# Kernel tuning notes

Measured on AMD Instinct MI355X. Metric: run time of the kernel, lower is better.

The kernel has to match this reference:

```python
import jax, jax.numpy as jnp
import numpy as np

B, S, SD, CD, F, H = 64, 2048, 32, 8, 1024, 512
D = CD + 1  # lstm input size


def _uinit(k, shape, fan_in):
    lim = 1.0 / np.sqrt(fan_in)
    return jax.random.uniform(k, shape, minval=-lim, maxval=lim, dtype=jnp.float32)


def setup_inputs() -> dict:
    key = jax.random.key(0)
    ks = jax.random.split(key, 12)
    return {
        "initial_state": jax.random.normal(ks[0], (B, SD), dtype=jnp.float32),
        "rnn_input": jax.random.normal(ks[1], (B, S, D), dtype=jnp.float32),
        # encoder MLP: in->H, H->H, H->F (equinox MLP depth=2, relu hidden, identity final)
        "enc_w0": _uinit(ks[2], (H, SD), SD), "enc_b0": _uinit(ks[3], (H,), SD),
        "enc_w1": _uinit(ks[4], (H, H), H), "enc_b1": _uinit(ks[5], (H,), H),
        "enc_w2": _uinit(ks[6], (F, H), H), "enc_b2": _uinit(ks[7], (F,), H),
        # equinox LSTMCell params: weight_ih (4F,D), weight_hh (4F,F), bias (4F,)
        "w_ih": _uinit(ks[8], (4 * F, D), F), "w_hh": _uinit(ks[9], (4 * F, F), F),
        "bias": _uinit(ks[10], (4 * F,), F),
    }


def reference(initial_state, rnn_input, enc_w0, enc_b0, enc_w1, enc_b1, enc_w2, enc_b2, w_ih, w_hh, bias):
    # encoder MLP -> initial hidden state
    h0 = jax.nn.relu(initial_state @ enc_w0.T + enc_b0)
    h0 = jax.nn.relu(h0 @ enc_w1.T + enc_b1)
    h0 = h0 @ enc_w2.T + enc_b2              # [B, F]
    c0 = jnp.zeros_like(h0)

    xs = jnp.swapaxes(rnn_input, 0, 1)       # [S, B, D]

    def step(carry, x):
        h, c = carry
        lin = x @ w_ih.T + h @ w_hh.T + bias  # [B, 4F]
        i, f, g, o = jnp.split(lin, 4, axis=-1)
        c_new = jax.nn.sigmoid(f) * c + jax.nn.sigmoid(i) * jnp.tanh(g)
        h_new = jax.nn.sigmoid(o) * jnp.tanh(c_new)
        # emit the PRE-step hidden state, matching `(self.cell(input, state), state[0])`
        return (h_new, c_new), h

    (h_last, _), h_seq = jax.lax.scan(step, (h0, c0), xs)
    return h_last, jnp.swapaxes(h_seq, 0, 1)  # [B,F], [B,S,F]
```

## Files before the change

kernel.cpp:

```cpp
#include <hip/hip_runtime.h>
#include <hip/hip_bf16.h>
#include <cstdint>
#include <cstddef>


typedef __bf16 bf16x8_t __attribute__((ext_vector_type(8)));
typedef float f32x4_t __attribute__((ext_vector_type(4)));
typedef int   i32x4_t __attribute__((ext_vector_type(4)));
typedef unsigned long long u64_t;
typedef unsigned long long u64x2_t __attribute__((ext_vector_type(2)));
typedef unsigned short u16x4_t __attribute__((ext_vector_type(4)));

#define WS_TAGS    0
#define WS_HBUF    1048576
#define WS_WSHUF   1310720
#define WS_WAUG    9699328
#define WS_XHAT    9961472
#define WS_H1      18350080
#define WS_H2      18481152

__device__ __forceinline__ unsigned short f2bf(float f) {
  unsigned int u = __float_as_uint(f);
  u = (u + 0x7fffu + ((u >> 16) & 1u)) >> 16;
  return (unsigned short)u;
}
__device__ __forceinline__ float sigm(float x) { return 1.f / (1.f + __expf(-x)); }
__device__ __forceinline__ float tanh_f(float x) {
  float e = __expf(-2.f * fabsf(x));
  float r = (1.f - e) / (1.f + e);
  return copysignf(r, x);
}


__global__ void flumen_enc1(const float* __restrict__ x, const float* __restrict__ W,
                            const float* __restrict__ b, float* __restrict__ h1) {
  const int bb = blockIdx.x;
  const int o  = threadIdx.x;
  const f32x4_t* xr = (const f32x4_t*)(x + bb * 32);
  const f32x4_t* wr = (const f32x4_t*)(W + o * 32);
  float acc = b[o];
#pragma unroll
  for (int q = 0; q < 8; ++q) {
    f32x4_t xv = xr[q], wv = wr[q];
    acc += xv[0] * wv[0] + xv[1] * wv[1] + xv[2] * wv[2] + xv[3] * wv[3];
  }
  h1[bb * 512 + o] = fmaxf(acc, 0.f);
}

__global__ void flumen_enc2(const float* __restrict__ in, const float* __restrict__ W,
                            const float* __restrict__ bv, float* __restrict__ outb) {
  __shared__ float s[64 * 256];
  const int tid = threadIdx.x;
  const int ol = tid & 63, bg = tid >> 6;
  const int o = blockIdx.x * 64 + ol;
  float bias = bv[o];
  float acc[8];
#pragma unroll
  for (int q = 0; q < 8; ++q) acc[q] = bias;
  for (int p = 0; p < 2; ++p) {
    __syncthreads();
    for (int i = tid; i < 4096; i += 512) {
      int flat = i * 4;
      int bb = flat >> 8, kk = flat & 255;
      *(f32x4_t*)(s + flat) = *(const f32x4_t*)(in + bb * 512 + p * 256 + kk);
    }
    __syncthreads();
    for (int kk = 0; kk < 256; kk += 4) {
      f32x4_t wv = *(const f32x4_t*)(W + o * 512 + p * 256 + kk);
#pragma unroll
      for (int j = 0; j < 4; ++j) {
        float wj = wv[j];
#pragma unroll
        for (int q = 0; q < 8; ++q)
          acc[q] += wj * s[(bg * 8 + q) * 256 + kk + j];
      }
    }
  }
#pragma unroll
  for (int q = 0; q < 8; ++q)
    outb[(bg * 8 + q) * 512 + o] = fmaxf(acc[q], 0.f);
}

__global__ void flumen_enc3(const float* __restrict__ in, const float* __restrict__ W,
                            const float* __restrict__ bv, float* __restrict__ dout,
                            unsigned short* __restrict__ hbuf) {
  __shared__ float s[64 * 256];
  const int tid = threadIdx.x;
  const int ol = tid & 63, bg = tid >> 6;
  const int o = blockIdx.x * 64 + ol;
  float bias = bv[o];
  float acc[8];
#pragma unroll
  for (int q = 0; q < 8; ++q) acc[q] = bias;
  for (int p = 0; p < 2; ++p) {
    __syncthreads();
    for (int i = tid; i < 4096; i += 512) {
      int flat = i * 4;
      int bb = flat >> 8, kk = flat & 255;
      *(f32x4_t*)(s + flat) = *(const f32x4_t*)(in + bb * 512 + p * 256 + kk);
    }
    __syncthreads();
    for (int kk = 0; kk < 256; kk += 4) {
      f32x4_t wv = *(const f32x4_t*)(W + o * 512 + p * 256 + kk);
#pragma unroll
      for (int j = 0; j < 4; ++j) {
        float wj = wv[j];
#pragma unroll
        for (int q = 0; q < 8; ++q)
          acc[q] += wj * s[(bg * 8 + q) * 256 + kk + j];
      }
    }
  }
  float* out_hseq = dout + 65536;
#pragma unroll
  for (int q = 0; q < 8; ++q) {
    int bb = bg * 8 + q;
    float v = acc[q];
    out_hseq[(size_t)bb * 2097152 + o] = v;
    int blk  = (bb >> 4) * 32 + (o >> 5);
    int lane = ((o >> 3) & 3) * 16 + (bb & 15);
    hbuf[blk * 512 + lane * 8 + (o & 7)] = f2bf(v);
  }
}


__global__ void flumen_wshuf(const float* __restrict__ src, unsigned short* __restrict__ dst) {
  int idx = blockIdx.x * 512 + threadIdx.x;
  int lane = idx & 63, kt = (idx >> 6) & 31, mt = idx >> 11;
  int r = lane & 15;
  int g = r & 3, f = mt * 4 + (r >> 2);
  int k0 = kt * 32 + (lane >> 4) * 8;
  const float* sp = src + (size_t)(g * 1024 + f) * 1024 + k0;
  f32x4_t v0 = *(const f32x4_t*)(sp);
  f32x4_t v1 = *(const f32x4_t*)(sp + 4);
  u16x4_t o0, o1;
#pragma unroll
  for (int j = 0; j < 4; ++j) { o0[j] = f2bf(v0[j]); o1[j] = f2bf(v1[j]); }
  u16x4_t* dp = (u16x4_t*)(dst + (size_t)idx * 8);
  dp[0] = o0; dp[1] = o1;
}

__global__ void flumen_waugi(const float* __restrict__ wih, const float* __restrict__ bias,
                             unsigned short* __restrict__ dst) {
  int idx = blockIdx.x * 512 + threadIdx.x;
  int lane = idx & 63, mt = idx >> 6;
  int r = lane & 15;
  int g = r & 3, f = mt * 4 + (r >> 2);
  int k0 = (lane >> 4) * 8;
  unsigned short o[8];
#pragma unroll
  for (int j = 0; j < 8; ++j) {
    int k = k0 + j;
    float v = (k < 9) ? wih[(size_t)(g * 1024 + f) * 9 + k]
                      : (k == 9 ? bias[g * 1024 + f] : 0.f);
    o[j] = f2bf(v);
  }
  u16x4_t* dp = (u16x4_t*)(dst + (size_t)idx * 8);
  dp[0] = *(u16x4_t*)&o[0];
  dp[1] = *(u16x4_t*)&o[4];
}

__global__ void flumen_convx(const float* __restrict__ xin, unsigned short* __restrict__ dst) {
  int i = (blockIdx.x * 512 + threadIdx.x) * 4;
  int b = i >> 16, t = (i >> 5) & 2047, c0 = i & 31;
  u16x4_t o;
#pragma unroll
  for (int j = 0; j < 4; ++j) {
    int cc = c0 + j;
    float v = (cc < 9) ? xin[((size_t)b * 2048 + t) * 9 + cc] : (cc == 9 ? 1.f : 0.f);
    o[j] = f2bf(v);
  }
  *(u16x4_t*)(dst + ((size_t)t * 64 + b) * 32 + c0) = o;
}

__global__ __launch_bounds__(512, 1) void flumen_lstm(
    const unsigned short* __restrict__ Wshuf,
    const unsigned short* __restrict__ WaugI,
    const unsigned short* __restrict__ Xhat,
    unsigned short* hbuf, int* tags, float* out)
{
  __shared__ __align__(16) char smem[140288];
  char*  h_lds = smem;
  float* hs    = (float*)(smem + 131072);
  float* pbuf  = (float*)smem;

  float* out_hlast = out;
  float* out_hseq  = out + 65536;
  const int w    = blockIdx.x;
  const int tid  = threadIdx.x;
  const int lane = tid & 63;
  const int wave = tid >> 6;
  const int mtp  = wave & 3;
  const int kh   = wave >> 2;
  const int l15  = lane & 15;
  const int l4   = lane >> 4;

  bf16x8_t Apin[2][16];
#pragma unroll
  for (int mtl = 0; mtl < 2; ++mtl) {
    const char* ap = (const char*)Wshuf + (size_t)(w * 8 + mtp * 2 + mtl) * 32768
                   + (size_t)(kh * 16) * 1024 + lane * 16;
#pragma unroll
    for (int k16 = 0; k16 < 16; ++k16)
      Apin[mtl][k16] = *(const bf16x8_t*)(ap + k16 * 1024);
  }
  bf16x8_t wfragI[2];
#pragma unroll
  for (int mtl = 0; mtl < 2; ++mtl)
    wfragI[mtl] = *(const bf16x8_t*)((const char*)WaugI
                                     + (size_t)(w * 8 + mtp * 2 + mtl) * 1024 + lane * 16);

  float carr[2][4] = {{0.f,0.f,0.f,0.f},{0.f,0.f,0.f,0.f}};

  for (int t = 0; t < 2048; ++t) {
    f32x4_t acc[2][4];
    if (kh == 0) {
#pragma unroll
      for (int n = 0; n < 4; ++n) {
        const int batch = n * 16 + l15;
        bf16x8_t xf = *(const bf16x8_t*)(Xhat + ((size_t)t * 64 + batch) * 32 + l4 * 8);
#pragma unroll
        for (int mtl = 0; mtl < 2; ++mtl)
          acc[mtl][n] = __builtin_amdgcn_mfma_f32_16x16x32_bf16(
              wfragI[mtl], xf, (f32x4_t){0.f, 0.f, 0.f, 0.f}, 0, 0, 0);
      }
    } else {
#pragma unroll
      for (int mtl = 0; mtl < 2; ++mtl)
#pragma unroll
        for (int n = 0; n < 4; ++n)
          acc[mtl][n] = (f32x4_t){0.f, 0.f, 0.f, 0.f};
    }

    if (t > 0) {
      if (lane < 32) {
        const char* tp = (const char*)tags + ((size_t)(t - 1) * 32 + lane) * 16;
        int iter = 0;
        while (true) {
          i32x4_t tv;
          asm volatile("global_load_dwordx4 %0, %1, off sc1\n\ts_waitcnt vmcnt(0)"
                       : "=v"(tv) : "v"(tp) : "memory");
          bool good = (tv[0] == t) && (tv[1] == t) && (tv[2] == t) && (tv[3] == t);
          if (__all(good) || ++iter >= (1 << 20)) break;
        }
      }
      __builtin_amdgcn_sched_barrier(0);
    }

    {
      const char* src0 = (const char*)hbuf + (size_t)((t & 1) * 131072) + tid * 16;
      f32x4_t v[8];
#pragma unroll
      for (int i = 0; i < 8; ++i)
        asm volatile("global_load_dwordx4 %0, %1, off sc1"
                     : "=v"(v[i]) : "v"(src0 + i * 8192) : "memory");
      asm volatile("s_waitcnt vmcnt(0)" ::: "memory");
      __builtin_amdgcn_sched_barrier(0);
#pragma unroll
      for (int i = 0; i < 8; ++i)
        *(f32x4_t*)(h_lds + tid * 16 + i * 8192) = v[i];
#pragma unroll
      for (int i = 0; i < 8; ++i)
        asm volatile("global_load_dwordx4 %0, %1, off sc1"
                     : "=v"(v[i]) : "v"(src0 + (i + 8) * 8192) : "memory");
      asm volatile("s_waitcnt vmcnt(0)" ::: "memory");
      __builtin_amdgcn_sched_barrier(0);
#pragma unroll
      for (int i = 0; i < 8; ++i)
        *(f32x4_t*)(h_lds + tid * 16 + (i + 8) * 8192) = v[i];
    }
    __syncthreads();

#pragma unroll
    for (int n = 0; n < 4; ++n) {
      const char* bb = h_lds + (size_t)(n * 32 + kh * 16) * 1024 + lane * 16;
#pragma unroll
      for (int k16 = 0; k16 < 16; ++k16) {
        bf16x8_t bf = *(const bf16x8_t*)(bb + k16 * 1024);
        acc[0][n] = __builtin_amdgcn_mfma_f32_16x16x32_bf16(Apin[0][k16], bf, acc[0][n], 0, 0, 0);
        acc[1][n] = __builtin_amdgcn_mfma_f32_16x16x32_bf16(Apin[1][k16], bf, acc[1][n], 0, 0, 0);
      }
    }
    __syncthreads();

    if (kh == 1) {
#pragma unroll
      for (int mtl = 0; mtl < 2; ++mtl)
#pragma unroll
        for (int n = 0; n < 4; ++n)
          *(f32x4_t*)(pbuf + ((size_t)((mtp * 8 + mtl * 4 + n) * 64) + lane) * 4)
              = acc[mtl][n];
    }
    __syncthreads();

    if (kh == 0) {
#pragma unroll
      for (int mtl = 0; mtl < 2; ++mtl)
#pragma unroll
        for (int n = 0; n < 4; ++n) {
          f32x4_t p = *(const f32x4_t*)(pbuf + ((size_t)((mtp * 8 + mtl * 4 + n) * 64) + lane) * 4);
          f32x4_t s = acc[mtl][n] + p;
          const int batch = n * 16 + l15;
          float c = sigm(s[1]) * carr[mtl][n] + sigm(s[0]) * tanh_f(s[2]);
          carr[mtl][n] = c;
          float h = sigm(s[3]) * tanh_f(c);
          const int fl = (mtp * 2 + mtl) * 4 + l4;
          if (t < 2047) {
            hs[batch * 36 + fl] = h;
          } else {
            out_hlast[batch * 1024 + w * 32 + fl] = h;
          }
        }
    }
    __syncthreads();

    if (t < 2047) {
      if (kh == 1) {
        const int b = mtp * 16 + l15;
        const float* hp = hs + b * 36 + l4 * 8;
        f32x4_t u0 = *(const f32x4_t*)(hp);
        f32x4_t u1 = *(const f32x4_t*)(hp + 4);
        u64_t lo = (u64_t)f2bf(u0[0]) | ((u64_t)f2bf(u0[1]) << 16)
                 | ((u64_t)f2bf(u0[2]) << 32) | ((u64_t)f2bf(u0[3]) << 48);
        u64_t hi = (u64_t)f2bf(u1[0]) | ((u64_t)f2bf(u1[1]) << 16)
                 | ((u64_t)f2bf(u1[2]) << 32) | ((u64_t)f2bf(u1[3]) << 48);
        u64x2_t qv = {lo, hi};
        char* dst = (char*)hbuf + (size_t)(((t + 1) & 1) * 131072)
                  + (size_t)(mtp * 32 + w) * 1024 + lane * 16;
        asm volatile("global_store_dwordx4 %0, %1, off sc1" :: "v"(dst), "v"(qv) : "memory");
        asm volatile("s_waitcnt vmcnt(0)" ::: "memory");
        if (lane == 0) {
          int val = t + 1;
          char* tp = (char*)tags + ((size_t)t * 32 + w) * 16 + mtp * 4;
          asm volatile("global_store_dword %0, %1, off sc1" :: "v"(tp), "v"(val) : "memory");
        }
      } else {
        const int b2 = mtp * 16 + (lane >> 2), sg = lane & 3;
        float* hd = out_hseq + ((size_t)b2 * 2048 + (size_t)(t + 1)) * 1024 + w * 32 + sg * 8;
        *(f32x4_t*)hd       = *(const f32x4_t*)(hs + b2 * 36 + sg * 8);
        *(f32x4_t*)(hd + 4) = *(const f32x4_t*)(hs + b2 * 36 + sg * 8 + 4);
      }
    }
  }
}


extern "C" void kernel_launch(void* const* d_in, const int* in_sizes, int n_in,
                              void* d_out, int out_size, void* d_ws, size_t ws_size,
                              hipStream_t stream) {
  const float* initial_state = (const float*)d_in[0];
  const float* rnn_input     = (const float*)d_in[1];
  const float* enc_w0        = (const float*)d_in[2];
  const float* enc_b0        = (const float*)d_in[3];
  const float* enc_w1        = (const float*)d_in[4];
  const float* enc_b1        = (const float*)d_in[5];
  const float* enc_w2        = (const float*)d_in[6];
  const float* enc_b2        = (const float*)d_in[7];
  const float* w_ih          = (const float*)d_in[8];
  const float* w_hh          = (const float*)d_in[9];
  const float* bias          = (const float*)d_in[10];

  char* ws = (char*)d_ws;
  int*            tags  = (int*)(ws + WS_TAGS);
  unsigned short* hbuf  = (unsigned short*)(ws + WS_HBUF);
  unsigned short* Wshuf = (unsigned short*)(ws + WS_WSHUF);
  unsigned short* WaugI = (unsigned short*)(ws + WS_WAUG);
  unsigned short* Xhat  = (unsigned short*)(ws + WS_XHAT);
  float*          h1    = (float*)(ws + WS_H1);
  float*          h2    = (float*)(ws + WS_H2);
  float*          out   = (float*)d_out;

  (void)hipMemsetAsync(tags, 0, 1048576, stream);
  flumen_enc1<<<64, 512, 0, stream>>>(initial_state, enc_w0, enc_b0, h1);
  flumen_enc2<<<8, 512, 0, stream>>>(h1, enc_w1, enc_b1, h2);
  flumen_enc3<<<16, 512, 0, stream>>>(h2, enc_w2, enc_b2, out, hbuf);
  flumen_wshuf<<<1024, 512, 0, stream>>>(w_hh, Wshuf);
  flumen_waugi<<<32, 512, 0, stream>>>(w_ih, bias, WaugI);
  flumen_convx<<<2048, 512, 0, stream>>>(rnn_input, Xhat);
  flumen_lstm<<<32, 512, 0, stream>>>(Wshuf, WaugI, Xhat, hbuf, tags, out);
}
```

Before: 18.40 ms.

## Replace tag flags with parity-encoded h data and pipeline per batch group

Removes the separate tag array and its polling: each block now spins directly on the hidden-state data, whose validity comes from a parity bit pattern XORed into the bf16 values (bit 14 flipped on alternating step pairs), and a scrub kernel pre-fills the buffers. The recurrent step is split into four 16-batch chunks, and the next chunk's h load is issued before the current chunk's MFMAs to overlap latency. This avoids a store-then-flag round trip and the waitcnt before the flag store, at the cost of more barriers per step and a validity check that depends on real h values never matching the sentinel bits.

```diff
diff --git a/kernel.cpp b/kernel.cpp
--- a/kernel.cpp
+++ b/kernel.cpp
@@ -6,18 +6,19 @@
 
 typedef __bf16 bf16x8_t __attribute__((ext_vector_type(8)));
 typedef float f32x4_t __attribute__((ext_vector_type(4)));
-typedef int   i32x4_t __attribute__((ext_vector_type(4)));
+typedef unsigned int u32x4_t __attribute__((ext_vector_type(4)));
 typedef unsigned long long u64_t;
 typedef unsigned long long u64x2_t __attribute__((ext_vector_type(2)));
 typedef unsigned short u16x4_t __attribute__((ext_vector_type(4)));
 
-#define WS_TAGS    0
-#define WS_HBUF    1048576
-#define WS_WSHUF   1310720
-#define WS_WAUG    9699328
-#define WS_XHAT    9961472
-#define WS_H1      18350080
-#define WS_H2      18481152
+#define WS_HBUF    0
+#define WS_WSHUF   393216
+#define WS_WAUG    8781824
+#define WS_XHAT    9043968
+#define WS_H1      17432576
+#define WS_H2      17563648
+
+#define PAR_M 0x40004000u
 
 __device__ __forceinline__ unsigned short f2bf(float f) {
   unsigned int u = __float_as_uint(f);
@@ -123,6 +124,12 @@
   }
 }
 
+
+__global__ void flumen_scrub(unsigned int* __restrict__ hb) {
+  int i = blockIdx.x * 512 + threadIdx.x;
+  u32x4_t pat = {PAR_M, 0u, PAR_M, 0u};
+  *(u32x4_t*)(hb + 32768 + i * 4) = pat;
+}
 
 __global__ void flumen_wshuf(const float* __restrict__ src, unsigned short* __restrict__ dst) {
   int idx = blockIdx.x * 512 + threadIdx.x;
@@ -177,12 +184,12 @@
     const unsigned short* __restrict__ Wshuf,
     const unsigned short* __restrict__ WaugI,
     const unsigned short* __restrict__ Xhat,
-    unsigned short* hbuf, int* tags, float* out)
+    unsigned short* hbuf, float* out)
 {
-  __shared__ __align__(16) char smem[140288];
+  __shared__ __align__(16) char smem[148480];
   char*  h_lds = smem;
   float* hs    = (float*)(smem + 131072);
-  float* pbuf  = (float*)smem;
+  float* pbuf  = (float*)(smem + 140288);
 
   float* out_hlast = out;
   float* out_hseq  = out + 65536;
@@ -212,133 +219,131 @@
 
   float carr[2][4] = {{0.f,0.f,0.f,0.f},{0.f,0.f,0.f,0.f}};
 
+  u32x4_t v[4];
+  {
+    const char* src = (const char*)hbuf + tid * 16;
+#pragma unroll
+    for (int i = 0; i < 4; ++i)
+      asm volatile("global_load_dwordx4 %0, %1, off sc1"
+                   : "=v"(v[i]) : "v"(src + i * 8192) : "memory");
+  }
+
   for (int t = 0; t < 2048; ++t) {
-    f32x4_t acc[2][4];
-    if (kh == 0) {
-#pragma unroll
-      for (int n = 0; n < 4; ++n) {
-        const int batch = n * 16 + l15;
-        bf16x8_t xf = *(const bf16x8_t*)(Xhat + ((size_t)t * 64 + batch) * 32 + l4 * 8);
-#pragma unroll
-        for (int mtl = 0; mtl < 2; ++mtl)
-          acc[mtl][n] = __builtin_amdgcn_mfma_f32_16x16x32_bf16(
-              wfragI[mtl], xf, (f32x4_t){0.f, 0.f, 0.f, 0.f}, 0, 0, 0);
-      }
-    } else {
-#pragma unroll
-      for (int mtl = 0; mtl < 2; ++mtl)
-#pragma unroll
-        for (int n = 0; n < 4; ++n)
-          acc[mtl][n] = (f32x4_t){0.f, 0.f, 0.f, 0.f};
-    }
-
-    if (t > 0) {
-      if (lane < 32) {
-        const char* tp = (const char*)tags + ((size_t)(t - 1) * 32 + lane) * 16;
+    const unsigned p  = (unsigned)((t >> 1) & 1);
+    const bool checkp = (t > 0);
+    const unsigned pm = (checkp && p) ? PAR_M : 0u;
+
+    for (int j = 0; j < 4; ++j) {
+      asm volatile("s_waitcnt vmcnt(0)" ::: "memory");
+      if (checkp) {
+        const char* src = (const char*)hbuf + (size_t)(131072 * (1 + (t & 1)))
+                        + j * 32768 + tid * 16;
         int iter = 0;
         while (true) {
-          i32x4_t tv;
-          asm volatile("global_load_dwordx4 %0, %1, off sc1\n\ts_waitcnt vmcnt(0)"
-                       : "=v"(tv) : "v"(tp) : "memory");
-          bool good = (tv[0] == t) && (tv[1] == t) && (tv[2] == t) && (tv[3] == t);
-          if (__all(good) || ++iter >= (1 << 20)) break;
+          unsigned a = 0xFFFFFFFFu, o = 0u;
+#pragma unroll
+          for (int i = 0; i < 4; ++i)
+#pragma unroll
+            for (int d = 0; d < 4; ++d) { a &= v[i][d]; o |= v[i][d]; }
+          bool valid = p ? ((a & PAR_M) == PAR_M) : ((o & PAR_M) == 0u);
+          if (__all(valid) || ++iter >= (1 << 18)) break;
+#pragma unroll
+          for (int i = 0; i < 4; ++i)
+            asm volatile("global_load_dwordx4 %0, %1, off sc1"
+                         : "=v"(v[i]) : "v"(src + i * 8192) : "memory");
+          asm volatile("s_waitcnt vmcnt(0)" ::: "memory");
         }
       }
       __builtin_amdgcn_sched_barrier(0);
-    }
-
-    {
-      const char* src0 = (const char*)hbuf + (size_t)((t & 1) * 131072) + tid * 16;
-      f32x4_t v[8];
-#pragma unroll
-      for (int i = 0; i < 8; ++i)
-        asm volatile("global_load_dwordx4 %0, %1, off sc1"
-                     : "=v"(v[i]) : "v"(src0 + i * 8192) : "memory");
-      asm volatile("s_waitcnt vmcnt(0)" ::: "memory");
-      __builtin_amdgcn_sched_barrier(0);
-#pragma unroll
-      for (int i = 0; i < 8; ++i)
-        *(f32x4_t*)(h_lds + tid * 16 + i * 8192) = v[i];
-#pragma unroll
-      for (int i = 0; i < 8; ++i)
-        asm volatile("global_load_dwordx4 %0, %1, off sc1"
-                     : "=v"(v[i]) : "v"(src0 + (i + 8) * 8192) : "memory");
-      asm volatile("s_waitcnt vmcnt(0)" ::: "memory");
-      __builtin_amdgcn_sched_barrier(0);
-#pragma unroll
-      for (int i = 0; i < 8; ++i)
-        *(f32x4_t*)(h_lds + tid * 16 + (i + 8) * 8192) = v[i];
-    }
-    __syncthreads();
-
-#pragma unroll
-    for (int n = 0; n < 4; ++n) {
-      const char* bb = h_lds + (size_t)(n * 32 + kh * 16) * 1024 + lane * 16;
-#pragma unroll
-      for (int k16 = 0; k16 < 16; ++k16) {
-        bf16x8_t bf = *(const bf16x8_t*)(bb + k16 * 1024);
-        acc[0][n] = __builtin_amdgcn_mfma_f32_16x16x32_bf16(Apin[0][k16], bf, acc[0][n], 0, 0, 0);
-        acc[1][n] = __builtin_amdgcn_mfma_f32_16x16x32_bf16(Apin[1][k16], bf, acc[1][n], 0, 0, 0);
-      }
-    }
-    __syncthreads();
-
-    if (kh == 1) {
-#pragma unroll
-      for (int mtl = 0; mtl < 2; ++mtl)
-#pragma unroll
-        for (int n = 0; n < 4; ++n)
-          *(f32x4_t*)(pbuf + ((size_t)((mtp * 8 + mtl * 4 + n) * 64) + lane) * 4)
-              = acc[mtl][n];
-    }
-    __syncthreads();
-
-    if (kh == 0) {
-#pragma unroll
-      for (int mtl = 0; mtl < 2; ++mtl)
-#pragma unroll
-        for (int n = 0; n < 4; ++n) {
-          f32x4_t p = *(const f32x4_t*)(pbuf + ((size_t)((mtp * 8 + mtl * 4 + n) * 64) + lane) * 4);
-          f32x4_t s = acc[mtl][n] + p;
-          const int batch = n * 16 + l15;
-          float c = sigm(s[1]) * carr[mtl][n] + sigm(s[0]) * tanh_f(s[2]);
-          carr[mtl][n] = c;
+      {
+        u32x4_t pmv = {pm, pm, pm, pm};
+#pragma unroll
+        for (int i = 0; i < 4; ++i)
+          *(u32x4_t*)(h_lds + j * 32768 + tid * 16 + i * 8192) = v[i] ^ pmv;
+      }
+      __syncthreads();
+
+      if (!(t == 2047 && j == 3)) {
+        const int tn = (j == 3) ? t + 1 : t;
+        const int jn = (j + 1) & 3;
+        const char* src = (const char*)hbuf
+            + (tn == 0 ? (size_t)0 : (size_t)(131072 * (1 + (tn & 1))))
+            + jn * 32768 + tid * 16;
+#pragma unroll
+        for (int i = 0; i < 4; ++i)
+          asm volatile("global_load_dwordx4 %0, %1, off sc1"
+                       : "=v"(v[i]) : "v"(src + i * 8192) : "memory");
+      }
+
+      f32x4_t acc[2];
+      if (kh == 0) {
+        bf16x8_t xf = *(const bf16x8_t*)(Xhat + ((size_t)t * 64 + j * 16 + l15) * 32 + l4 * 8);
+#pragma unroll
+        for (int mtl = 0; mtl < 2; ++mtl)
+          acc[mtl] = __builtin_amdgcn_mfma_f32_16x16x32_bf16(
+              wfragI[mtl], xf, (f32x4_t){0.f, 0.f, 0.f, 0.f}, 0, 0, 0);
+      } else {
+        acc[0] = (f32x4_t){0.f, 0.f, 0.f, 0.f};
+        acc[1] = (f32x4_t){0.f, 0.f, 0.f, 0.f};
+      }
+      {
+        const char* bb = h_lds + j * 32768 + (size_t)(kh * 16) * 1024 + lane * 16;
+#pragma unroll
+        for (int k16 = 0; k16 < 16; ++k16) {
+          bf16x8_t bf = *(const bf16x8_t*)(bb + k16 * 1024);
+          acc[0] = __builtin_amdgcn_mfma_f32_16x16x32_bf16(Apin[0][k16], bf, acc[0], 0, 0, 0);
+          acc[1] = __builtin_amdgcn_mfma_f32_16x16x32_bf16(Apin[1][k16], bf, acc[1], 0, 0, 0);
+        }
+      }
+      if (kh == 1) {
+#pragma unroll
+        for (int mtl = 0; mtl < 2; ++mtl)
+          *(f32x4_t*)(pbuf + (size_t)((mtp * 2 + mtl) * 64 + lane) * 4) = acc[mtl];
+      }
+      __syncthreads();
+
+      if (kh == 0) {
+#pragma unroll
+        for (int mtl = 0; mtl < 2; ++mtl) {
+          f32x4_t pt = *(const f32x4_t*)(pbuf + (size_t)((mtp * 2 + mtl) * 64 + lane) * 4);
+          f32x4_t s = acc[mtl] + pt;
+          float c = sigm(s[1]) * carr[mtl][j] + sigm(s[0]) * tanh_f(s[2]);
+          carr[mtl][j] = c;
           float h = sigm(s[3]) * tanh_f(c);
           const int fl = (mtp * 2 + mtl) * 4 + l4;
           if (t < 2047) {
-            hs[batch * 36 + fl] = h;
+            hs[(j * 16 + l15) * 36 + fl] = h;
           } else {
-            out_hlast[batch * 1024 + w * 32 + fl] = h;
+            out_hlast[(j * 16 + l15) * 1024 + w * 32 + fl] = h;
           }
         }
-    }
-    __syncthreads();
-
-    if (t < 2047) {
-      if (kh == 1) {
-        const int b = mtp * 16 + l15;
-        const float* hp = hs + b * 36 + l4 * 8;
-        f32x4_t u0 = *(const f32x4_t*)(hp);
-        f32x4_t u1 = *(const f32x4_t*)(hp + 4);
-        u64_t lo = (u64_t)f2bf(u0[0]) | ((u64_t)f2bf(u0[1]) << 16)
-                 | ((u64_t)f2bf(u0[2]) << 32) | ((u64_t)f2bf(u0[3]) << 48);
-        u64_t hi = (u64_t)f2bf(u1[0]) | ((u64_t)f2bf(u1[1]) << 16)
-                 | ((u64_t)f2bf(u1[2]) << 32) | ((u64_t)f2bf(u1[3]) << 48);
-        u64x2_t qv = {lo, hi};
-        char* dst = (char*)hbuf + (size_t)(((t + 1) & 1) * 131072)
-                  + (size_t)(mtp * 32 + w) * 1024 + lane * 16;
-        asm volatile("global_store_dwordx4 %0, %1, off sc1" :: "v"(dst), "v"(qv) : "memory");
-        asm volatile("s_waitcnt vmcnt(0)" ::: "memory");
-        if (lane == 0) {
-          int val = t + 1;
-          char* tp = (char*)tags + ((size_t)t * 32 + w) * 16 + mtp * 4;
-          asm volatile("global_store_dword %0, %1, off sc1" :: "v"(tp), "v"(val) : "memory");
+      }
+      __syncthreads();
+
+      if (t < 2047) {
+        if (wave == 4) {
+          const int b = j * 16 + l15;
+          const float* hp = hs + b * 36 + l4 * 8;
+          f32x4_t u0 = *(const f32x4_t*)(hp);
+          f32x4_t u1 = *(const f32x4_t*)(hp + 4);
+          u64_t lo = (u64_t)f2bf(u0[0]) | ((u64_t)f2bf(u0[1]) << 16)
+                   | ((u64_t)f2bf(u0[2]) << 32) | ((u64_t)f2bf(u0[3]) << 48);
+          u64_t hi = (u64_t)f2bf(u1[0]) | ((u64_t)f2bf(u1[1]) << 16)
+                   | ((u64_t)f2bf(u1[2]) << 32) | ((u64_t)f2bf(u1[3]) << 48);
+          if (((t + 1) >> 1) & 1) {
+            lo ^= 0x4000400040004000ULL;
+            hi ^= 0x4000400040004000ULL;
+          }
+          u64x2_t qv = {lo, hi};
+          char* dst = (char*)hbuf + (size_t)(131072 * (1 + ((t + 1) & 1)))
+                    + (size_t)(j * 32 + w) * 1024 + lane * 16;
+          asm volatile("global_store_dwordx4 %0, %1, off sc1" :: "v"(dst), "v"(qv) : "memory");
+        } else if (wave == 5 || wave == 6) {
+          const int idx = (wave - 5) * 64 + lane;
+          const int b2 = j * 16 + (idx >> 3), sg = idx & 7;
+          float* hd = out_hseq + ((size_t)b2 * 2048 + (size_t)(t + 1)) * 1024 + w * 32 + sg * 4;
+          *(f32x4_t*)hd = *(const f32x4_t*)(hs + b2 * 36 + sg * 4);
         }
-      } else {
-        const int b2 = mtp * 16 + (lane >> 2), sg = lane & 3;
-        float* hd = out_hseq + ((size_t)b2 * 2048 + (size_t)(t + 1)) * 1024 + w * 32 + sg * 8;
-        *(f32x4_t*)hd       = *(const f32x4_t*)(hs + b2 * 36 + sg * 8);
-        *(f32x4_t*)(hd + 4) = *(const f32x4_t*)(hs + b2 * 36 + sg * 8 + 4);
       }
     }
   }
@@ -361,7 +366,6 @@
   const float* bias          = (const float*)d_in[10];
 
   char* ws = (char*)d_ws;
-  int*            tags  = (int*)(ws + WS_TAGS);
   unsigned short* hbuf  = (unsigned short*)(ws + WS_HBUF);
   unsigned short* Wshuf = (unsigned short*)(ws + WS_WSHUF);
   unsigned short* WaugI = (unsigned short*)(ws + WS_WAUG);
@@ -370,12 +374,12 @@
   float*          h2    = (float*)(ws + WS_H2);
   float*          out   = (float*)d_out;
 
-  (void)hipMemsetAsync(tags, 0, 1048576, stream);
+  flumen_scrub<<<32, 512, 0, stream>>>((unsigned int*)hbuf);
   flumen_enc1<<<64, 512, 0, stream>>>(initial_state, enc_w0, enc_b0, h1);
   flumen_enc2<<<8, 512, 0, stream>>>(h1, enc_w1, enc_b1, h2);
   flumen_enc3<<<16, 512, 0, stream>>>(h2, enc_w2, enc_b2, out, hbuf);
   flumen_wshuf<<<1024, 512, 0, stream>>>(w_hh, Wshuf);
   flumen_waugi<<<32, 512, 0, stream>>>(w_ih, bias, WaugI);
   flumen_convx<<<2048, 512, 0, stream>>>(rnn_input, Xhat);
-  flumen_lstm<<<32, 512, 0, stream>>>(Wshuf, WaugI, Xhat, hbuf, tags, out);
-}
+  flumen_lstm<<<32, 512, 0, stream>>>(Wshuf, WaugI, Xhat, hbuf, out);
+}
```

Measured after the change: 18.80 ms. +2.2%, slower.
